# Kernel optimization log

Measured on AMD Instinct MI355X. Metric: run time of the kernel, lower is better.

The kernel has to match this reference:

```python
import jax, jax.numpy as jnp
import numpy as np

WS, SS, IMG, NH = 7, 3, 56, 6  # window, shift, image size, heads
N = WS * WS                    # tokens per window = 49


def _rel_pos_index():
    coords = np.stack(np.meshgrid(np.arange(WS), np.arange(WS), indexing='ij')).reshape(2, -1)
    rel = (coords[:, :, None] - coords[:, None, :]).transpose(1, 2, 0)  # (N,N,2)
    rel[..., 0] += WS - 1
    rel[..., 1] += WS - 1
    rel[..., 0] *= 2 * WS - 1
    return rel.sum(-1)  # (N,N) int


def _attn_mask():
    m = np.zeros((IMG, IMG), np.float32)
    sl = (slice(0, -WS), slice(-WS, -SS), slice(-SS, None))
    cnt = 0
    for hs in sl:
        for ws_ in sl:
            m[hs, ws_] = cnt
            cnt += 1
    mw = m.reshape(IMG // WS, WS, IMG // WS, WS).transpose(0, 2, 1, 3).reshape(-1, N)  # (nW,N)
    diff = mw[:, None, :] - mw[:, :, None]
    return np.where(diff != 0, -100.0, 0.0).astype(np.float32)  # (nW,N,N)


def _ln(x, g, b, eps=1e-5):
    mu = x.mean(-1, keepdims=True)
    var = ((x - mu) ** 2).mean(-1, keepdims=True)
    return (x - mu) * jax.lax.rsqrt(var + eps) * g + b


def reference(x, rpb_table, w_qkv, b_qkv, w_proj, b_proj, g0, be0, g1, be1, w_fc1, b_fc1, w_fc2, b_fc2):
    B, C, _, _ = x.shape
    dh = C // NH
    nWs = IMG // WS
    nW = nWs * nWs

    xs = x.transpose(0, 2, 3, 1)            # NHWC [B,IMG,IMG,C]
    shortcut = xs
    h = _ln(xs, g0, be0)
    h = jnp.roll(h, (-SS, -SS), axis=(1, 2))
    # window partition -> [B*nW, N, C]
    h = h.reshape(B, nWs, WS, nWs, WS, C).transpose(0, 1, 3, 2, 4, 5).reshape(B * nW, N, C)

    qkv = h @ w_qkv.T + b_qkv               # [B_,N,3C]
    qkv = qkv.reshape(B * nW, N, dh, NH, 3)  # matches torch reshape (b_,N,C//h,h,3)
    q = qkv[..., 0].transpose(0, 3, 1, 2) * (dh ** -0.5)  # [B_,H,N,dh]
    k = qkv[..., 1].transpose(0, 3, 1, 2)
    v = qkv[..., 2].transpose(0, 3, 1, 2)

    att = jnp.einsum('bhnd,bhmd->bhnm', q, k)             # [B_,H,N,N]
    bias = rpb_table[jnp.asarray(_rel_pos_index().reshape(-1))].reshape(N, N, NH).transpose(2, 0, 1)
    att = att + bias[None]
    mask = jnp.asarray(_attn_mask())                      # [nW,N,N]
    att = att.reshape(B, nW, NH, N, N) + mask[None, :, None]
    att = jax.nn.softmax(att.reshape(B * nW, NH, N, N), axis=-1)

    o = jnp.einsum('bhnm,bhmd->bnhd', att, v).reshape(B * nW, WS, WS, C)
    o = o @ w_proj.T + b_proj
    # window reverse -> [B,IMG,IMG,C]
    o = o.reshape(B, nWs, nWs, WS, WS, C).transpose(0, 1, 3, 2, 4, 5).reshape(B, IMG, IMG, C)
    o = jnp.roll(o, (SS, SS), axis=(1, 2))

    xs = shortcut + o
    h2 = _ln(xs, g1, be1)
    h2 = jax.nn.gelu(h2 @ w_fc1.T + b_fc1, approximate=False) @ w_fc2.T + b_fc2
    xs = xs + h2
    return xs.transpose(0, 3, 1, 2)  # back to NCHW


def setup_inputs() -> dict:
    key = jax.random.key(0)
    ks = jax.random.split(key, 8)
    C, Hn = 192, 768
    return {
        'x': jax.random.normal(ks[0], (64, C, 56, 56), jnp.float32),
        'rpb_table': jax.random.normal(ks[1], (169, NH), jnp.float32) * 0.02,
        'w_qkv': jax.random.normal(ks[2], (3 * C, C), jnp.float32) * 0.02,
        'b_qkv': jnp.zeros((3 * C,), jnp.float32),
        'w_proj': jax.random.normal(ks[3], (C, C), jnp.float32) * 0.02,
        'b_proj': jnp.zeros((C,), jnp.float32),
        'g0': jnp.ones((C,), jnp.float32),
        'be0': jnp.zeros((C,), jnp.float32),
        'g1': jnp.ones((C,), jnp.float32),
        'be1': jnp.zeros((C,), jnp.float32),
        'w_fc1': jax.random.normal(ks[4], (Hn, C), jnp.float32) * 0.02,
        'b_fc1': jnp.zeros((Hn,), jnp.float32),
        'w_fc2': jax.random.normal(ks[5], (C, Hn), jnp.float32) * 0.02,
        'b_fc2': jnp.zeros((C,), jnp.float32),
    }
```

## Files before the change

kernel.cpp:

```cpp
#include <hip/hip_runtime.h>
#include <hip/hip_bf16.h>

typedef unsigned short ushortT;
typedef __attribute__((ext_vector_type(8))) short short8;
typedef __attribute__((ext_vector_type(4))) float f32x4;
typedef __attribute__((address_space(3))) unsigned int lds_uint;
typedef __attribute__((address_space(1))) const unsigned int glob_uint;

#define MFMA16(a,b,c) __builtin_amdgcn_mfma_f32_16x16x32_bf16(a,b,c,0,0,0)

__device__ __forceinline__ ushortT f2bf(float f){
  union {float f; unsigned u;} v; v.f = f;
  unsigned r = v.u + 0x7FFFu + ((v.u >> 16) & 1u);
  return (ushortT)(r >> 16);
}
__device__ __forceinline__ float bf2f(ushortT u){
  union {unsigned u; float f;} v; v.u = ((unsigned)u) << 16; return v.f;
}
__device__ __forceinline__ float gelu_f(float v){
  float u = 0.7978845608028654f * (v + 0.044715f*v*v*v);
  float e = __expf(2.0f*u);
  return 0.5f * v * (1.0f + (1.0f - 2.0f/(e + 1.0f)));
}

#define SCALE_Q 0.17677669529663687f

__global__ void k_prep(const float* __restrict__ rpb, const float* __restrict__ wqkv,
                       const float* __restrict__ bqkv, const float* __restrict__ wproj,
                       const float* __restrict__ wfc1, const float* __restrict__ wfc2,
                       ushortT* __restrict__ wqkvp, float* __restrict__ bqkvp,
                       ushortT* __restrict__ wprojb, ushortT* __restrict__ wfc1b,
                       ushortT* __restrict__ wfc2b, float* __restrict__ bm)
{
  int i = blockIdx.x * 256 + threadIdx.x;
  if (i < 110592){
    int rp = i / 192, c = i % 192;
    int s = rp / 192, rem = rp % 192, hh = rem / 32, d = rem % 32;
    int rin = d*18 + hh*3 + s;
    float v = wqkv[rin*192 + c];
    if (s == 0) v *= SCALE_Q;
    wqkvp[i] = f2bf(v);
    return;
  }
  i -= 110592;
  if (i < 576){
    int rp = i;
    int s = rp / 192, rem = rp % 192, hh = rem / 32, d = rem % 32;
    int rin = d*18 + hh*3 + s;
    float v = bqkv[rin];
    if (s == 0) v *= SCALE_Q;
    bqkvp[i] = v;
    return;
  }
  i -= 576;
  if (i < 36864){ wprojb[i] = f2bf(wproj[i]); return; }
  i -= 36864;
  if (i < 147456){ wfc1b[i] = f2bf(wfc1[i]); return; }
  i -= 147456;
  if (i < 147456){ wfc2b[i] = f2bf(wfc2[i]); return; }
  i -= 147456;
  if (i < 921984){
    int j = i % 49; int t = i / 49; int ii = t % 49; t /= 49; int hh = t % 6; int w = t / 6;
    int r1 = ii/7, c1 = ii%7, r2 = j/7, c2 = j%7;
    int idx = (r1 - r2 + 6)*13 + (c1 - c2 + 6);
    float bias = rpb[idx*6 + hh];
    int wy = w >> 3, wx = w & 7;
    int hi = wy*7 + r1, wi = wx*7 + c1, hj = wy*7 + r2, wj = wx*7 + c2;
    int regi = 3*((hi<49)?0:((hi<53)?1:2)) + ((wi<49)?0:((wi<53)?1:2));
    int regj = 3*((hj<49)?0:((hj<53)?1:2)) + ((wj<49)?0:((wj<53)?1:2));
    bm[i] = bias + ((regi != regj) ? -100.0f : 0.0f);
  }
}

__global__ void k_tr(const float* __restrict__ x, ushortT* __restrict__ xsb)
{
  __shared__ float tile[192*57];
  int bh = blockIdx.x; int b = bh / 56, h = bh % 56;
  const float* src = x + (size_t)b*602112 + (size_t)h*56;
  for (int e = threadIdx.x; e < 192*56; e += 256){
    int c = e / 56, w = e % 56;
    tile[c*57 + w] = src[(size_t)c*3136 + w];
  }
  __syncthreads();
  ushortT* dst = xsb + (size_t)bh*56*192;
  for (int e = threadIdx.x; e < 56*192; e += 256){
    int w = e / 192, c = e % 192;
    dst[(size_t)w*192 + c] = f2bf(tile[c*57 + w]);
  }
}

__global__ __launch_bounds__(256,3) void k_attn(
  ushortT* __restrict__ xsb, const ushortT* __restrict__ wqkvp, const float* __restrict__ bqkvp,
  const ushortT* __restrict__ wprojb, const float* __restrict__ bproj,
  const float* __restrict__ g0, const float* __restrict__ be0,
  const float* __restrict__ g1, const float* __restrict__ be1,
  const float* __restrict__ bm, ushortT* __restrict__ xs2b)
{
  __shared__ ushortT ln0[49][200];
  __shared__ ushortT ksh[49][104];
  __shared__ ushortT vTh[3][32][72];
  __shared__ ushortT Pw[4][16][72];

  const int tid = threadIdx.x;
  const int lane = tid & 63, wv = tid >> 6;
  const int l15 = lane & 15, g = lane >> 4;
  const int wid = blockIdx.x;
  const int b = wid >> 6, wloc = wid & 63, wy = wloc >> 3, wx = wloc & 7;
  const int mbase = wv * 16;

  for (int t = wv; t < 49; t += 4){
    int r = t / 7, cc = t % 7;
    int hsrc = (wy*7 + r + 3) % 56;
    int wsrc = (wx*7 + cc + 3) % 56;
    const ushortT* px = xsb + ((size_t)((b*56 + hsrc)*56 + wsrc))*192;
    float x0 = bf2f(px[lane]), x1 = bf2f(px[lane+64]), x2 = bf2f(px[lane+128]);
    float s = x0 + x1 + x2, sq = x0*x0 + x1*x1 + x2*x2;
    #pragma unroll
    for (int m = 1; m < 64; m <<= 1){ s += __shfl_xor(s, m, 64); sq += __shfl_xor(sq, m, 64); }
    float mu = s * (1.0f/192.0f);
    float var = sq * (1.0f/192.0f) - mu*mu;
    float rs = rsqrtf(var + 1e-5f);
    ln0[t][lane]     = f2bf((x0-mu)*rs*g0[lane]     + be0[lane]);
    ln0[t][lane+64]  = f2bf((x1-mu)*rs*g0[lane+64]  + be0[lane+64]);
    ln0[t][lane+128] = f2bf((x2-mu)*rs*g0[lane+128] + be0[lane+128]);
  }
  __syncthreads();

  short8 a[4][6];
  #pragma unroll
  for (int mt = 0; mt < 4; mt++){
    int ra = mt*16 + l15; if (ra > 48) ra = 48;
    #pragma unroll
    for (int kc = 0; kc < 6; kc++)
      a[mt][kc] = *(const short8*)(&ln0[ra][kc*32 + g*8]);
  }
  __syncthreads();

  for (int ntl = 0; ntl < 6; ntl++){
    int idx = wv*6 + ntl;
    int nt = (idx < 18) ? idx : idx + 6;
    int cp = nt*16 + l15;
    const ushortT* wp = wqkvp + (size_t)cp*192 + g*8;
    short8 bfr[6];
    #pragma unroll
    for (int kc = 0; kc < 6; kc++) bfr[kc] = *(const short8*)(wp + kc*32);
    float bias = bqkvp[cp];
    #pragma unroll
    for (int mt = 0; mt < 4; mt++){
      f32x4 acc = {0.f,0.f,0.f,0.f};
      #pragma unroll
      for (int kc = 0; kc < 6; kc++) acc = MFMA16(a[mt][kc], bfr[kc], acc);
      #pragma unroll
      for (int r = 0; r < 4; r++){
        int tok = mt*16 + g*4 + r;
        float v = acc[r] + bias;
        if (cp < 192)      { if (tok < 49) ln0[tok][cp] = f2bf(v); }
        else if (cp < 384) { if (tok < 49) ksh[tok][cp-192] = f2bf(v); }
        else { int c2 = cp - 384; vTh[c2>>5][c2&31][tok] = f2bf(v); }
      }
    }
  }
  __syncthreads();

  const int rq = (mbase + l15 > 48) ? 48 : (mbase + l15);
  for (int hl = 0; hl < 3; hl++){
    int h = hl;
    float bmv[4][4];
    #pragma unroll
    for (int r = 0; r < 4; r++){
      int i = mbase + g*4 + r;
      int ic = (i < 49) ? i : 48;
      const float* bmrow = bm + (((size_t)(wloc*6 + h)*49 + ic)*49);
      #pragma unroll
      for (int jt = 0; jt < 4; jt++){
        int j = jt*16 + l15;
        bmv[r][jt] = (i < 49 && j < 49) ? bmrow[j] : -1e30f;
      }
    }
    short8 aq = *(const short8*)(&ln0[rq][h*32 + g*8]);
    f32x4 sreg[4];
    #pragma unroll
    for (int jt = 0; jt < 4; jt++){
      int rk = jt*16 + l15; if (rk > 48) rk = 48;
      short8 bk = *(const short8*)(&ksh[rk][hl*32 + g*8]);
      f32x4 z = {0.f,0.f,0.f,0.f};
      sreg[jt] = MFMA16(aq, bk, z);
    }
    #pragma unroll
    for (int r = 0; r < 4; r++){
      float rv[4];
      #pragma unroll
      for (int jt = 0; jt < 4; jt++){
        float bmvv = bmv[r][jt];
        rv[jt] = (bmvv < -1e29f) ? -1e30f : sreg[jt][r] + bmvv;
      }
      float mx = fmaxf(fmaxf(rv[0],rv[1]), fmaxf(rv[2],rv[3]));
      #pragma unroll
      for (int m = 1; m < 16; m <<= 1) mx = fmaxf(mx, __shfl_xor(mx, m, 64));
      float sum = 0.f;
      #pragma unroll
      for (int jt = 0; jt < 4; jt++){ rv[jt] = __expf(rv[jt] - mx); sum += rv[jt]; }
      #pragma unroll
      for (int m = 1; m < 16; m <<= 1) sum += __shfl_xor(sum, m, 64);
      float rden = 1.0f / sum;
      #pragma unroll
      for (int jt = 0; jt < 4; jt++)
        Pw[wv][g*4+r][jt*16 + l15] = f2bf(rv[jt] * rden);
    }
    #pragma unroll
    for (int nt2 = 0; nt2 < 2; nt2++){
      f32x4 oacc = {0.f,0.f,0.f,0.f};
      #pragma unroll
      for (int kk = 0; kk < 2; kk++){
        short8 ap = *(const short8*)(&Pw[wv][l15][kk*32 + g*8]);
        short8 bv = *(const short8*)(&vTh[hl][nt2*16 + l15][kk*32 + g*8]);
        oacc = MFMA16(ap, bv, oacc);
      }
      #pragma unroll
      for (int r = 0; r < 4; r++){
        int tok = mbase + g*4 + r;
        if (tok < 49) ln0[tok][h*32 + nt2*16 + l15] = f2bf(oacc[r]);
      }
    }
  }
  __syncthreads();

  for (int ntl = 0; ntl < 3; ntl++){
    int idx = wv*3 + ntl;
    int nt = (idx < 6) ? 18 + idx : 24 + idx;
    int cp = nt*16 + l15;
    const ushortT* wp = wqkvp + (size_t)cp*192 + g*8;
    short8 bfr[6];
    #pragma unroll
    for (int kc = 0; kc < 6; kc++) bfr[kc] = *(const short8*)(wp + kc*32);
    float bias = bqkvp[cp];
    #pragma unroll
    for (int mt = 0; mt < 4; mt++){
      f32x4 acc = {0.f,0.f,0.f,0.f};
      #pragma unroll
      for (int kc = 0; kc < 6; kc++) acc = MFMA16(a[mt][kc], bfr[kc], acc);
      #pragma unroll
      for (int r = 0; r < 4; r++){
        int tok = mt*16 + g*4 + r;
        float v = acc[r] + bias;
        if (cp < 384) { if (tok < 49) ksh[tok][cp-288] = f2bf(v); }
        else { int c2 = cp - 480; vTh[c2>>5][c2&31][tok] = f2bf(v); }
      }
    }
  }
  __syncthreads();

  for (int hl = 0; hl < 3; hl++){
    int h = 3 + hl;
    float bmv[4][4];
    #pragma unroll
    for (int r = 0; r < 4; r++){
      int i = mbase + g*4 + r;
      int ic = (i < 49) ? i : 48;
      const float* bmrow = bm + (((size_t)(wloc*6 + h)*49 + ic)*49);
      #pragma unroll
      for (int jt = 0; jt < 4; jt++){
        int j = jt*16 + l15;
        bmv[r][jt] = (i < 49 && j < 49) ? bmrow[j] : -1e30f;
      }
    }
    short8 aq = *(const short8*)(&ln0[rq][h*32 + g*8]);
    f32x4 sreg[4];
    #pragma unroll
    for (int jt = 0; jt < 4; jt++){
      int rk = jt*16 + l15; if (rk > 48) rk = 48;
      short8 bk = *(const short8*)(&ksh[rk][hl*32 + g*8]);
      f32x4 z = {0.f,0.f,0.f,0.f};
      sreg[jt] = MFMA16(aq, bk, z);
    }
    #pragma unroll
    for (int r = 0; r < 4; r++){
      float rv[4];
      #pragma unroll
      for (int jt = 0; jt < 4; jt++){
        float bmvv = bmv[r][jt];
        rv[jt] = (bmvv < -1e29f) ? -1e30f : sreg[jt][r] + bmvv;
      }
      float mx = fmaxf(fmaxf(rv[0],rv[1]), fmaxf(rv[2],rv[3]));
      #pragma unroll
      for (int m = 1; m < 16; m <<= 1) mx = fmaxf(mx, __shfl_xor(mx, m, 64));
      float sum = 0.f;
      #pragma unroll
      for (int jt = 0; jt < 4; jt++){ rv[jt] = __expf(rv[jt] - mx); sum += rv[jt]; }
      #pragma unroll
      for (int m = 1; m < 16; m <<= 1) sum += __shfl_xor(sum, m, 64);
      float rden = 1.0f / sum;
      #pragma unroll
      for (int jt = 0; jt < 4; jt++)
        Pw[wv][g*4+r][jt*16 + l15] = f2bf(rv[jt] * rden);
    }
    #pragma unroll
    for (int nt2 = 0; nt2 < 2; nt2++){
      f32x4 oacc = {0.f,0.f,0.f,0.f};
      #pragma unroll
      for (int kk = 0; kk < 2; kk++){
        short8 ap = *(const short8*)(&Pw[wv][l15][kk*32 + g*8]);
        short8 bv = *(const short8*)(&vTh[hl][nt2*16 + l15][kk*32 + g*8]);
        oacc = MFMA16(ap, bv, oacc);
      }
      #pragma unroll
      for (int r = 0; r < 4; r++){
        int tok = mbase + g*4 + r;
        if (tok < 49) ln0[tok][h*32 + nt2*16 + l15] = f2bf(oacc[r]);
      }
    }
  }
  __syncthreads();

  {
    short8 a2[4][6];
    #pragma unroll
    for (int mt = 0; mt < 4; mt++){
      int ra = mt*16 + l15; if (ra > 48) ra = 48;
      #pragma unroll
      for (int kc = 0; kc < 6; kc++)
        a2[mt][kc] = *(const short8*)(&ln0[ra][kc*32 + g*8]);
    }
    __syncthreads();
    #pragma unroll
    for (int ntl = 0; ntl < 3; ntl++){
      int nt = wv*3 + ntl;
      int cp = nt*16 + l15;
      const ushortT* wp = wprojb + (size_t)cp*192 + g*8;
      short8 bfr[6];
      #pragma unroll
      for (int kc = 0; kc < 6; kc++) bfr[kc] = *(const short8*)(wp + kc*32);
      #pragma unroll
      for (int mt = 0; mt < 4; mt++){
        f32x4 acc = {0.f,0.f,0.f,0.f};
        #pragma unroll
        for (int kc = 0; kc < 6; kc++) acc = MFMA16(a2[mt][kc], bfr[kc], acc);
        #pragma unroll
        for (int r = 0; r < 4; r++){
          int tok = mt*16 + g*4 + r;
          if (tok < 49) ln0[tok][cp] = f2bf(acc[r]);
        }
      }
    }
  }
  __syncthreads();

  for (int t = wv; t < 49; t += 4){
    int rr = t / 7, cc = t % 7;
    int hdst = (wy*7 + rr + 3) % 56, wdst = (wx*7 + cc + 3) % 56;
    size_t gtok = ((size_t)(b*56 + hdst)*56 + wdst)*192;
    float v0 = bf2f(ln0[t][lane])     + bproj[lane]     + bf2f(xsb[gtok + lane]);
    float v1 = bf2f(ln0[t][lane+64])  + bproj[lane+64]  + bf2f(xsb[gtok + lane+64]);
    float v2 = bf2f(ln0[t][lane+128]) + bproj[lane+128] + bf2f(xsb[gtok + lane+128]);
    float s = v0 + v1 + v2, sq = v0*v0 + v1*v1 + v2*v2;
    #pragma unroll
    for (int m = 1; m < 64; m <<= 1){ s += __shfl_xor(s, m, 64); sq += __shfl_xor(sq, m, 64); }
    float mu = s * (1.0f/192.0f);
    float var = sq * (1.0f/192.0f) - mu*mu;
    float rs = rsqrtf(var + 1e-5f);
    xs2b[gtok + lane]     = f2bf(v0);
    xs2b[gtok + lane+64]  = f2bf(v1);
    xs2b[gtok + lane+128] = f2bf(v2);
    xsb[gtok + lane]     = f2bf((v0-mu)*rs*g1[lane]     + be1[lane]);
    xsb[gtok + lane+64]  = f2bf((v1-mu)*rs*g1[lane+64]  + be1[lane+64]);
    xsb[gtok + lane+128] = f2bf((v2-mu)*rs*g1[lane+128] + be1[lane+128]);
  }
}

__global__ __launch_bounds__(512,4) void k_mlp_fused(
  const ushortT* __restrict__ A,
  const ushortT* __restrict__ w1g,
  const float* __restrict__ b1,
  const ushortT* __restrict__ w2g,
  const float* __restrict__ b2,
  const ushortT* __restrict__ xs2b,
  float* __restrict__ out)
{
  __shared__ ushortT w1s[2][6144];
  __shared__ ushortT w2s[2][6144];
  __shared__ ushortT Hbuf[128][40];

  const int tid = threadIdx.x, lane = tid & 63, wv = tid >> 6;
  const int l15 = lane & 15, g = lane >> 4;
  const size_t Mbase = (size_t)blockIdx.x * 128;
  const int rowb = wv * 16;

  short8 a[6];
  {
    size_t row = Mbase + rowb + l15;
    #pragma unroll
    for (int kc = 0; kc < 6; kc++)
      a[kc] = __builtin_nontemporal_load((const short8*)(A + row*192 + kc*32 + g*8));
  }

  #define STAGE(HB, NB)                                                         \
    _Pragma("unroll")                                                           \
    for (int j = 0; j < 3; j++){                                                \
      int id = wv + j*8;                                                        \
      if (id < 12){                                                             \
        int ci = id;                                                            \
        int q = ci*4 + (lane >> 4);                                             \
        int gq = q & 3, t = q >> 2;                                             \
        int nt = t / 6, kc = t % 6;                                             \
        const ushortT* src = w1g + (size_t)((HB)*32 + nt*16 + (lane & 15))*192  \
                             + kc*32 + gq*8;                                    \
        __builtin_amdgcn_global_load_lds((glob_uint*)src,                       \
            (lds_uint*)(&w1s[NB][ci*512]), 16, 0, 0);                           \
      } else {                                                                  \
        int ci = id - 12;                                                       \
        int q = ci*4 + (lane >> 4);                                             \
        int nt = q >> 2, gq = q & 3;                                            \
        const ushortT* src = w2g + (size_t)(nt*16 + (lane & 15))*768            \
                             + (HB)*32 + gq*8;                                  \
        __builtin_amdgcn_global_load_lds((glob_uint*)src,                       \
            (lds_uint*)(&w2s[NB][ci*512]), 16, 0, 0);                           \
      }                                                                         \
    }

  STAGE(0, 0);
  __syncthreads();

  f32x4 acc2[12];
  #pragma unroll
  for (int nt = 0; nt < 12; nt++) acc2[nt] = (f32x4){0.f,0.f,0.f,0.f};

  for (int hb = 0; hb < 24; hb++){
    const int cb = hb & 1;
    if (hb < 23){ STAGE(hb+1, cb^1); }

    #pragma unroll
    for (int nt = 0; nt < 2; nt++){
      short8 bfr[6];
      #pragma unroll
      for (int kc = 0; kc < 6; kc++){
        int q = (nt*6 + kc)*4 + g;
        bfr[kc] = *(const short8*)(&w1s[cb][(q*16 + l15)*8]);
      }
      float bias = b1[hb*32 + nt*16 + l15];
      f32x4 acc = {0.f,0.f,0.f,0.f};
      #pragma unroll
      for (int kc = 0; kc < 6; kc++) acc = MFMA16(a[kc], bfr[kc], acc);
      #pragma unroll
      for (int r = 0; r < 4; r++)
        Hbuf[rowb + g*4 + r][nt*16 + l15] = f2bf(gelu_f(acc[r] + bias));
    }
    short8 h2f = *(const short8*)(&Hbuf[rowb + l15][g*8]);
    #pragma unroll
    for (int nt = 0; nt < 12; nt++){
      int q2 = nt*4 + g;
      short8 wfr = *(const short8*)(&w2s[cb][(q2*16 + l15)*8]);
      acc2[nt] = MFMA16(h2f, wfr, acc2[nt]);
    }
    __syncthreads();
  }

  #pragma unroll
  for (int nt = 0; nt < 12; nt++){
    int c = nt*16 + l15;
    float bs = b2[c];
    #pragma unroll
    for (int r = 0; r < 4; r++){
      size_t tok = Mbase + rowb + g*4 + r;
      float v = acc2[nt][r] + bs + bf2f(xs2b[tok*192 + c]);
      unsigned t32 = (unsigned)tok;
      unsigned bb = t32 / 3136u, rem = t32 % 3136u;
      out[(size_t)bb*602112 + (size_t)c*3136 + rem] = v;
    }
  }
  #undef STAGE
}

extern "C" void kernel_launch(void* const* d_in, const int* in_sizes, int n_in,
                              void* d_out, int out_size, void* d_ws, size_t ws_size,
                              hipStream_t stream)
{
  const float* x      = (const float*)d_in[0];
  const float* rpb    = (const float*)d_in[1];
  const float* w_qkv  = (const float*)d_in[2];
  const float* b_qkv  = (const float*)d_in[3];
  const float* w_proj = (const float*)d_in[4];
  const float* b_proj = (const float*)d_in[5];
  const float* g0     = (const float*)d_in[6];
  const float* be0    = (const float*)d_in[7];
  const float* g1     = (const float*)d_in[8];
  const float* be1    = (const float*)d_in[9];
  const float* w_fc1  = (const float*)d_in[10];
  const float* b_fc1  = (const float*)d_in[11];
  const float* w_fc2  = (const float*)d_in[12];
  const float* b_fc2  = (const float*)d_in[13];
  float* out = (float*)d_out;
  char* ws = (char*)d_ws;

  ushortT* xsb    = (ushortT*)(ws);
  ushortT* xs2b   = (ushortT*)(ws + 77070336);
  ushortT* wqkvp  = (ushortT*)(ws + 154140672);
  float*   bqkvp  = (float*)(ws + 154361856);
  ushortT* wprojb = (ushortT*)(ws + 154364160);
  ushortT* wfc1b  = (ushortT*)(ws + 154437888);
  ushortT* wfc2b  = (ushortT*)(ws + 154732800);
  float*   bm     = (float*)(ws + 155027712);

  k_prep<<<5332, 256, 0, stream>>>(rpb, w_qkv, b_qkv, w_proj, w_fc1, w_fc2,
                                   wqkvp, bqkvp, wprojb, wfc1b, wfc2b, bm);
  k_tr<<<3584, 256, 0, stream>>>(x, xsb);
  k_attn<<<4096, 256, 0, stream>>>(xsb, wqkvp, bqkvp, wprojb, b_proj,
                                   g0, be0, g1, be1, bm, xs2b);
  k_mlp_fused<<<1568, 512, 0, stream>>>(xsb, wfc1b, b_fc1, wfc2b, b_fc2, xs2b, out);
}
```

Baseline: 687.3 us.

## Move LayerNorm0 into transpose kernel and load normalized A-fragments from global

The first LayerNorm now runs in the transpose kernel, which writes a second bf16 buffer of normalized activations. The attention kernel loads its QKV A-fragments straight from that buffer, in two places, instead of normalizing into shared memory, which removes an LDS pass and a barrier at the start. The cost is an extra 77MB global write plus re-reads in the attention kernel, and a larger workspace.

```diff
diff --git a/kernel.cpp b/kernel.cpp
--- a/kernel.cpp
+++ b/kernel.cpp
@@ -72,9 +72,12 @@
   }
 }
 
-__global__ void k_tr(const float* __restrict__ x, ushortT* __restrict__ xsb)
+__global__ __launch_bounds__(256,3) void k_tr(const float* __restrict__ x,
+    const float* __restrict__ g0, const float* __restrict__ be0,
+    ushortT* __restrict__ xsb, ushortT* __restrict__ ln0sb)
 {
   __shared__ float tile[192*57];
+  __shared__ float mu_s[56], rs_s[56];
   int bh = blockIdx.x; int b = bh / 56, h = bh % 56;
   const float* src = x + (size_t)b*602112 + (size_t)h*56;
   for (int e = threadIdx.x; e < 192*56; e += 256){
@@ -82,21 +85,39 @@
     tile[c*57 + w] = src[(size_t)c*3136 + w];
   }
   __syncthreads();
-  ushortT* dst = xsb + (size_t)bh*56*192;
+  {
+    int w = threadIdx.x >> 2, q = threadIdx.x & 3;
+    if (w < 56){
+      float s = 0.f, sq = 0.f;
+      #pragma unroll 8
+      for (int i = 0; i < 48; i++){ float v = tile[(q*48+i)*57 + w]; s += v; sq += v*v; }
+      s  += __shfl_xor(s, 1, 64);  sq += __shfl_xor(sq, 1, 64);
+      s  += __shfl_xor(s, 2, 64);  sq += __shfl_xor(sq, 2, 64);
+      if (q == 0){
+        float mu = s*(1.0f/192.0f), var = sq*(1.0f/192.0f) - mu*mu;
+        mu_s[w] = mu; rs_s[w] = rsqrtf(var + 1e-5f);
+      }
+    }
+  }
+  __syncthreads();
+  ushortT* dst  = xsb   + (size_t)bh*56*192;
+  ushortT* dstl = ln0sb + (size_t)bh*56*192;
   for (int e = threadIdx.x; e < 56*192; e += 256){
     int w = e / 192, c = e % 192;
-    dst[(size_t)w*192 + c] = f2bf(tile[c*57 + w]);
+    float v = tile[c*57 + w];
+    dst[(size_t)w*192 + c]  = f2bf(v);
+    dstl[(size_t)w*192 + c] = f2bf((v - mu_s[w])*rs_s[w]*g0[c] + be0[c]);
   }
 }
 
 __global__ __launch_bounds__(256,3) void k_attn(
-  ushortT* __restrict__ xsb, const ushortT* __restrict__ wqkvp, const float* __restrict__ bqkvp,
+  ushortT* __restrict__ xsb, const ushortT* __restrict__ ln0sb,
+  const ushortT* __restrict__ wqkvp, const float* __restrict__ bqkvp,
   const ushortT* __restrict__ wprojb, const float* __restrict__ bproj,
-  const float* __restrict__ g0, const float* __restrict__ be0,
   const float* __restrict__ g1, const float* __restrict__ be1,
   const float* __restrict__ bm, ushortT* __restrict__ xs2b)
 {
-  __shared__ ushortT ln0[49][200];
+  __shared__ ushortT qbuf[49][200];
   __shared__ ushortT ksh[49][104];
   __shared__ ushortT vTh[3][32][72];
   __shared__ ushortT Pw[4][16][72];
@@ -108,33 +129,18 @@
   const int b = wid >> 6, wloc = wid & 63, wy = wloc >> 3, wx = wloc & 7;
   const int mbase = wv * 16;
 
-  for (int t = wv; t < 49; t += 4){
-    int r = t / 7, cc = t % 7;
-    int hsrc = (wy*7 + r + 3) % 56;
-    int wsrc = (wx*7 + cc + 3) % 56;
-    const ushortT* px = xsb + ((size_t)((b*56 + hsrc)*56 + wsrc))*192;
-    float x0 = bf2f(px[lane]), x1 = bf2f(px[lane+64]), x2 = bf2f(px[lane+128]);
-    float s = x0 + x1 + x2, sq = x0*x0 + x1*x1 + x2*x2;
-    #pragma unroll
-    for (int m = 1; m < 64; m <<= 1){ s += __shfl_xor(s, m, 64); sq += __shfl_xor(sq, m, 64); }
-    float mu = s * (1.0f/192.0f);
-    float var = sq * (1.0f/192.0f) - mu*mu;
-    float rs = rsqrtf(var + 1e-5f);
-    ln0[t][lane]     = f2bf((x0-mu)*rs*g0[lane]     + be0[lane]);
-    ln0[t][lane+64]  = f2bf((x1-mu)*rs*g0[lane+64]  + be0[lane+64]);
-    ln0[t][lane+128] = f2bf((x2-mu)*rs*g0[lane+128] + be0[lane+128]);
-  }
-  __syncthreads();
-
   short8 a[4][6];
   #pragma unroll
   for (int mt = 0; mt < 4; mt++){
     int ra = mt*16 + l15; if (ra > 48) ra = 48;
+    int r = ra / 7, cc = ra % 7;
+    int hsrc = (wy*7 + r + 3) % 56;
+    int wsrc = (wx*7 + cc + 3) % 56;
+    const ushortT* px = ln0sb + ((size_t)((b*56 + hsrc)*56 + wsrc))*192 + g*8;
     #pragma unroll
     for (int kc = 0; kc < 6; kc++)
-      a[mt][kc] = *(const short8*)(&ln0[ra][kc*32 + g*8]);
-  }
-  __syncthreads();
+      a[mt][kc] = *(const short8*)(px + kc*32);
+  }
 
   for (int ntl = 0; ntl < 6; ntl++){
     int idx = wv*6 + ntl;
@@ -154,7 +160,7 @@
       for (int r = 0; r < 4; r++){
         int tok = mt*16 + g*4 + r;
         float v = acc[r] + bias;
-        if (cp < 192)      { if (tok < 49) ln0[tok][cp] = f2bf(v); }
+        if (cp < 192)      { if (tok < 49) qbuf[tok][cp] = f2bf(v); }
         else if (cp < 384) { if (tok < 49) ksh[tok][cp-192] = f2bf(v); }
         else { int c2 = cp - 384; vTh[c2>>5][c2&31][tok] = f2bf(v); }
       }
@@ -177,7 +183,7 @@
         bmv[r][jt] = (i < 49 && j < 49) ? bmrow[j] : -1e30f;
       }
     }
-    short8 aq = *(const short8*)(&ln0[rq][h*32 + g*8]);
+    short8 aq = *(const short8*)(&qbuf[rq][h*32 + g*8]);
     f32x4 sreg[4];
     #pragma unroll
     for (int jt = 0; jt < 4; jt++){
@@ -219,9 +225,22 @@
       #pragma unroll
       for (int r = 0; r < 4; r++){
         int tok = mbase + g*4 + r;
-        if (tok < 49) ln0[tok][h*32 + nt2*16 + l15] = f2bf(oacc[r]);
-      }
-    }
+        if (tok < 49) qbuf[tok][h*32 + nt2*16 + l15] = f2bf(oacc[r]);
+      }
+    }
+  }
+
+  short8 a1[4][6];
+  #pragma unroll
+  for (int mt = 0; mt < 4; mt++){
+    int ra = mt*16 + l15; if (ra > 48) ra = 48;
+    int r = ra / 7, cc = ra % 7;
+    int hsrc = (wy*7 + r + 3) % 56;
+    int wsrc = (wx*7 + cc + 3) % 56;
+    const ushortT* px = ln0sb + ((size_t)((b*56 + hsrc)*56 + wsrc))*192 + g*8;
+    #pragma unroll
+    for (int kc = 0; kc < 6; kc++)
+      a1[mt][kc] = *(const short8*)(px + kc*32);
   }
   __syncthreads();
 
@@ -238,7 +257,7 @@
     for (int mt = 0; mt < 4; mt++){
       f32x4 acc = {0.f,0.f,0.f,0.f};
       #pragma unroll
-      for (int kc = 0; kc < 6; kc++) acc = MFMA16(a[mt][kc], bfr[kc], acc);
+      for (int kc = 0; kc < 6; kc++) acc = MFMA16(a1[mt][kc], bfr[kc], acc);
       #pragma unroll
       for (int r = 0; r < 4; r++){
         int tok = mt*16 + g*4 + r;
@@ -264,7 +283,7 @@
         bmv[r][jt] = (i < 49 && j < 49) ? bmrow[j] : -1e30f;
       }
     }
-    short8 aq = *(const short8*)(&ln0[rq][h*32 + g*8]);
+    short8 aq = *(const short8*)(&qbuf[rq][h*32 + g*8]);
     f32x4 sreg[4];
     #pragma unroll
     for (int jt = 0; jt < 4; jt++){
@@ -306,7 +325,7 @@
       #pragma unroll
       for (int r = 0; r < 4; r++){
         int tok = mbase + g*4 + r;
-        if (tok < 49) ln0[tok][h*32 + nt2*16 + l15] = f2bf(oacc[r]);
+        if (tok < 49) qbuf[tok][h*32 + nt2*16 + l15] = f2bf(oacc[r]);
       }
     }
   }
@@ -319,7 +338,7 @@
       int ra = mt*16 + l15; if (ra > 48) ra = 48;
       #pragma unroll
       for (int kc = 0; kc < 6; kc++)
-        a2[mt][kc] = *(const short8*)(&ln0[ra][kc*32 + g*8]);
+        a2[mt][kc] = *(const short8*)(&qbuf[ra][kc*32 + g*8]);
     }
     __syncthreads();
     #pragma unroll
@@ -338,7 +357,7 @@
         #pragma unroll
         for (int r = 0; r < 4; r++){
           int tok = mt*16 + g*4 + r;
-          if (tok < 49) ln0[tok][cp] = f2bf(acc[r]);
+          if (tok < 49) qbuf[tok][cp] = f2bf(acc[r]);
         }
       }
     }
@@ -349,9 +368,9 @@
     int rr = t / 7, cc = t % 7;
     int hdst = (wy*7 + rr + 3) % 56, wdst = (wx*7 + cc + 3) % 56;
     size_t gtok = ((size_t)(b*56 + hdst)*56 + wdst)*192;
-    float v0 = bf2f(ln0[t][lane])     + bproj[lane]     + bf2f(xsb[gtok + lane]);
-    float v1 = bf2f(ln0[t][lane+64])  + bproj[lane+64]  + bf2f(xsb[gtok + lane+64]);
-    float v2 = bf2f(ln0[t][lane+128]) + bproj[lane+128] + bf2f(xsb[gtok + lane+128]);
+    float v0 = bf2f(qbuf[t][lane])     + bproj[lane]     + bf2f(xsb[gtok + lane]);
+    float v1 = bf2f(qbuf[t][lane+64])  + bproj[lane+64]  + bf2f(xsb[gtok + lane+64]);
+    float v2 = bf2f(qbuf[t][lane+128]) + bproj[lane+128] + bf2f(xsb[gtok + lane+128]);
     float s = v0 + v1 + v2, sq = v0*v0 + v1*v1 + v2*v2;
     #pragma unroll
     for (int m = 1; m < 64; m <<= 1){ s += __shfl_xor(s, m, 64); sq += __shfl_xor(sq, m, 64); }
@@ -492,18 +511,19 @@
   char* ws = (char*)d_ws;
 
   ushortT* xsb    = (ushortT*)(ws);
-  ushortT* xs2b   = (ushortT*)(ws + 77070336);
-  ushortT* wqkvp  = (ushortT*)(ws + 154140672);
-  float*   bqkvp  = (float*)(ws + 154361856);
-  ushortT* wprojb = (ushortT*)(ws + 154364160);
-  ushortT* wfc1b  = (ushortT*)(ws + 154437888);
-  ushortT* wfc2b  = (ushortT*)(ws + 154732800);
-  float*   bm     = (float*)(ws + 155027712);
+  ushortT* ln0sb  = (ushortT*)(ws + 77070336);
+  ushortT* xs2b   = (ushortT*)(ws + 154140672);
+  ushortT* wqkvp  = (ushortT*)(ws + 231211008);
+  float*   bqkvp  = (float*)(ws + 231432192);
+  ushortT* wprojb = (ushortT*)(ws + 231434496);
+  ushortT* wfc1b  = (ushortT*)(ws + 231508224);
+  ushortT* wfc2b  = (ushortT*)(ws + 231803136);
+  float*   bm     = (float*)(ws + 232098048);
 
   k_prep<<<5332, 256, 0, stream>>>(rpb, w_qkv, b_qkv, w_proj, w_fc1, w_fc2,
                                    wqkvp, bqkvp, wprojb, wfc1b, wfc2b, bm);
-  k_tr<<<3584, 256, 0, stream>>>(x, xsb);
-  k_attn<<<4096, 256, 0, stream>>>(xsb, wqkvp, bqkvp, wprojb, b_proj,
-                                   g0, be0, g1, be1, bm, xs2b);
+  k_tr<<<3584, 256, 0, stream>>>(x, g0, be0, xsb, ln0sb);
+  k_attn<<<4096, 256, 0, stream>>>(xsb, ln0sb, wqkvp, bqkvp, wprojb, b_proj,
+                                   g1, be1, bm, xs2b);
   k_mlp_fused<<<1568, 512, 0, stream>>>(xsb, wfc1b, b_fc1, wfc2b, b_fc2, xs2b, out);
 }
```

Measured after the change: 709.5 us. 1.03x slower.
